# Performance work log

Measured on AMD Instinct MI355X. Metric: run time of the kernel, lower is better.

Reference implementation:

```python
import jax, jax.numpy as jnp
import numpy as np

N = 10000      # atoms
E = 160000     # edges (avg degree 16)
H = 64         # hidden_channels
R = 64         # num_rbf
MAXZ = 100
RC = 4.5       # cutoff_upper (cutoff_lower = 0)
LN_EPS = 1e-5


def setup_inputs() -> dict:
    key = jax.random.key(0)
    ks = jax.random.split(key, 20)
    z = jax.random.randint(ks[0], (N,), 0, MAXZ, dtype=jnp.int32)
    edge_index = jax.random.randint(ks[1], (2, E), 0, N, dtype=jnp.int32)
    edge_weight = jax.random.uniform(ks[2], (E,), dtype=jnp.float32) * RC
    v = jax.random.normal(ks[3], (E, 3), dtype=jnp.float32)
    edge_vec_norm = v / jnp.linalg.norm(v, axis=-1, keepdims=True)
    edge_attr = jax.random.normal(ks[4], (E, R), dtype=jnp.float32)
    p = lambda k, shape: (jax.random.normal(k, shape, dtype=jnp.float32) * 0.1)
    return {
        'z': z, 'edge_index': edge_index, 'edge_weight': edge_weight,
        'edge_vec_norm': edge_vec_norm, 'edge_attr': edge_attr,
        'emb': p(ks[5], (MAXZ, H)),
        'emb2_w': p(ks[6], (H, 2 * H)), 'emb2_b': p(ks[7], (H,)),
        'dp1_w': p(ks[8], (H, R)), 'dp1_b': p(ks[9], (H,)),
        'dp2_w': p(ks[10], (H, R)), 'dp2_b': p(ks[11], (H,)),
        'dp3_w': p(ks[12], (H, R)), 'dp3_b': p(ks[13], (H,)),
        'ln_g': jnp.ones((H,), jnp.float32), 'ln_b': jnp.zeros((H,), jnp.float32),
        'w1': p(ks[14], (2 * H, H)), 'b1': jnp.zeros((2 * H,), jnp.float32),
        'w2': p(ks[15], (3 * H, 2 * H)), 'b2': jnp.zeros((3 * H,), jnp.float32),
        'm0': p(ks[16], (H, H)), 'm1': p(ks[17], (H, H)), 'm2': p(ks[18], (H, H)),
    }


def reference(z, edge_index, edge_weight, edge_vec_norm, edge_attr,
              emb, emb2_w, emb2_b, dp1_w, dp1_b, dp2_w, dp2_b, dp3_w, dp3_b,
              ln_g, ln_b, w1, b1, w2, b2, m0, m1, m2):
    n_atoms = z.shape[0]
    hc = emb.shape[1]
    src, dst = edge_index[0], edge_index[1]

    # atomic number message Z_ij: concat(Z_i, Z_j) -> Linear  [E,H]
    Zn = emb[z]
    Zij = jnp.concatenate([Zn[src], Zn[dst]], axis=-1) @ emb2_w.T + emb2_b

    # cosine cutoff (cutoff_lower == 0)
    C = 0.5 * (jnp.cos(edge_weight * jnp.pi / RC) + 1.0) * (edge_weight < RC)

    # RBF-gated per-edge channel weights, all [E,H]
    g1 = (edge_attr @ dp1_w.T + dp1_b) * C[:, None] * Zij
    g2 = (edge_attr @ dp2_w.T + dp2_b) * C[:, None] * Zij
    g3 = (edge_attr @ dp3_w.T + dp3_b) * C[:, None] * Zij

    eye = jnp.eye(3, dtype=Zij.dtype)
    vx, vy, vz = edge_vec_norm[:, 0], edge_vec_norm[:, 1], edge_vec_norm[:, 2]
    zero = jnp.zeros_like(vx)
    skew = jnp.stack([zero, -vz, vy, vz, zero, -vx, -vy, vx, zero], axis=-1).reshape(-1, 3, 3)
    outer = edge_vec_norm[:, :, None] * edge_vec_norm[:, None, :]  # [E,3,3], symmetric
    sym = outer - (jnp.trace(outer, axis1=-2, axis2=-1) / 3.0)[:, None, None] * eye

    # per-edge messages [E,H,3,3]
    Iij = g1[:, :, None, None] * eye
    Aij = g2[:, :, None, None] * skew[:, None, :, :]
    Sij = g3[:, :, None, None] * sym[:, None, :, :]

    # scatter-add to atoms
    I = jax.ops.segment_sum(Iij, src, num_segments=n_atoms)
    A = jax.ops.segment_sum(Aij, src, num_segments=n_atoms)
    S = jax.ops.segment_sum(Sij, src, num_segments=n_atoms)

    # tensor norm -> layernorm -> MLP1
    tn = ((I + A + S) ** 2).sum((-2, -1))  # [N,H]
    mu = tn.mean(-1, keepdims=True)
    var = ((tn - mu) ** 2).mean(-1, keepdims=True)
    norm = (tn - mu) / jnp.sqrt(var + LN_EPS) * ln_g + ln_b
    norm = jax.nn.silu(norm @ w1.T + b1)
    norm = jax.nn.silu(norm @ w2.T + b2)
    norm = norm.reshape(-1, hc, 3)
    n0 = norm[..., 0][:, :, None, None]

    # channel-mixing; NOTE: original code applies MLP2[1]/MLP2[2] to the
    # updated I and gates all three with norm[...,0] -- replicated faithfully.
    I = jnp.einsum('nhij,kh->nkij', I, m0) * n0
    A = jnp.einsum('nhij,kh->nkij', I, m1) * n0
    S = jnp.einsum('nhij,kh->nkij', I, m2) * n0
    return I + A + S
```

## Files before the change

kernel.cpp:

```cpp
#include <hip/hip_runtime.h>
#include <stdint.h>

#define NATOMS 10000
#define NEDGES 160000
#define RCUT   4.5f
#define CAP    64
#define ATGRID 1024

#define T_BYTES    ((size_t)NATOMS * 640 * 4)
#define CNT_OFF    (T_BYTES)
#define CNT_BYTES  ((size_t)NATOMS * 4)
#define REC_OFF    (CNT_OFF + CNT_BYTES)
#define REC_BYTES  ((size_t)NATOMS * CAP * 16)
#define EMB_OFF    (REC_OFF + REC_BYTES)
#define EMB_BYTES  ((size_t)100 * 64 * 2)

typedef unsigned short u16;
typedef __bf16 bf16x8 __attribute__((ext_vector_type(8)));
typedef float  f32x4  __attribute__((ext_vector_type(4)));

#define MFMA16(a,b,c) __builtin_amdgcn_mfma_f32_16x16x32_bf16((a),(b),(c),0,0,0)
#define BFMAGIC 0x3F803F80u
#define MSK 0xffff0000u

__device__ __forceinline__ float uf(unsigned int u){ return __uint_as_float(u); }
__device__ __forceinline__ float b2f(u16 u){
  union { unsigned int i; float f; } v; v.i = ((unsigned int)u) << 16; return v.f;
}
__device__ __forceinline__ u16 f2b(float f){
  union { unsigned int i; float f; } v; v.f = f;
  unsigned int b = v.i + 0x7fffu + ((v.i >> 16) & 1u);
  return (u16)(b >> 16);
}
__device__ __forceinline__ float ldf(const void* p, int i, int bf){
  if (bf) return b2f(((const u16*)p)[i]);
  return ((const float*)p)[i];
}
__device__ __forceinline__ bf16x8 ld8bf(const void* p, int i, int bf){
  if (bf) return *(const bf16x8*)((const u16*)p + i);
  const float4* q = (const float4*)((const float*)p + i);
  float4 a = q[0], b = q[1];
  bf16x8 r;
  r[0]=(__bf16)a.x; r[1]=(__bf16)a.y; r[2]=(__bf16)a.z; r[3]=(__bf16)a.w;
  r[4]=(__bf16)b.x; r[5]=(__bf16)b.y; r[6]=(__bf16)b.z; r[7]=(__bf16)b.w;
  return r;
}
__device__ __forceinline__ uint4 ld8pk(const void* p, int i, int bf){
  if (bf) return *(const uint4*)((const u16*)p + i);
  const float4* q = (const float4*)((const float*)p + i);
  float4 a = q[0], b = q[1];
  uint4 r;
  r.x = (unsigned int)f2b(a.x) | ((unsigned int)f2b(a.y) << 16);
  r.y = (unsigned int)f2b(a.z) | ((unsigned int)f2b(a.w) << 16);
  r.z = (unsigned int)f2b(b.x) | ((unsigned int)f2b(b.y) << 16);
  r.w = (unsigned int)f2b(b.z) | ((unsigned int)f2b(b.w) << 16);
  return r;
}
__device__ __forceinline__ void ld8f(const void* p, int i, float* o, int bf){
  if (bf){
    uint4 v = *(const uint4*)((const u16*)p + i);
    o[0]=uf(v.x<<16); o[1]=uf(v.x&MSK); o[2]=uf(v.y<<16); o[3]=uf(v.y&MSK);
    o[4]=uf(v.z<<16); o[5]=uf(v.z&MSK); o[6]=uf(v.w<<16); o[7]=uf(v.w&MSK);
    return;
  }
  const float4* q = (const float4*)((const float*)p + i);
  float4 a = q[0], b = q[1];
  o[0]=a.x; o[1]=a.y; o[2]=a.z; o[3]=a.w; o[4]=b.x; o[5]=b.y; o[6]=b.z; o[7]=b.w;
}
__device__ __forceinline__ uint4 pk8(const float* f){
  uint4 r;
  r.x = (unsigned int)f2b(f[0]) | ((unsigned int)f2b(f[1]) << 16);
  r.y = (unsigned int)f2b(f[2]) | ((unsigned int)f2b(f[3]) << 16);
  r.z = (unsigned int)f2b(f[4]) | ((unsigned int)f2b(f[5]) << 16);
  r.w = (unsigned int)f2b(f[6]) | ((unsigned int)f2b(f[7]) << 16);
  return r;
}

__global__ __launch_bounds__(256) void scatter_kernel(const int* __restrict__ ei,
                                                      const int* __restrict__ z,
                                                      const void* __restrict__ ew,
                                                      const void* __restrict__ evn,
                                                      const void* __restrict__ emb,
                                                      u16* __restrict__ emb16,
                                                      int* __restrict__ cnt,
                                                      uint4* __restrict__ REC,
                                                      const unsigned int* __restrict__ lng){
  const int bf = (lng[0] == BFMAGIC);
  int e = blockIdx.x * 256 + threadIdx.x;
  if (e < 6400) emb16[e] = bf ? ((const u16*)emb)[e] : f2b(((const float*)emb)[e]);
  int s = ei[e], d = ei[NEDGES + e];
  int p = atomicAdd(&cnt[s], 1);
  const float w  = ldf(ew, e, bf);
  const float Cv = (w < RCUT) ? 0.5f*(__cosf(w * (3.14159265358979f / RCUT)) + 1.0f) : 0.0f;
  uint4 rec;
  rec.x = (unsigned int)e;
  rec.y = (unsigned int)z[d];
  rec.z = (unsigned int)f2b(ldf(evn, 3*e + 0, bf)) | ((unsigned int)f2b(ldf(evn, 3*e + 1, bf)) << 16);
  rec.w = (unsigned int)f2b(ldf(evn, 3*e + 2, bf)) | ((unsigned int)f2b(Cv) << 16);
  if (p < CAP) REC[(size_t)s*CAP + p] = rec;
}

__global__ __launch_bounds__(256)
void atomT_kernel(
    const int* __restrict__ z,
    const u16* __restrict__ emb16,
    const void* __restrict__ attr,
    const uint4* __restrict__ REC,
    const int* __restrict__ cnt,
    const void* __restrict__ e2w, const void* __restrict__ e2b,
    const void* __restrict__ d1w, const void* __restrict__ d1b,
    const void* __restrict__ d2w, const void* __restrict__ d2b,
    const void* __restrict__ d3w, const void* __restrict__ d3b,
    float* __restrict__ T,
    const unsigned int* __restrict__ lng)
{
  __shared__ __align__(16) u16 dpW[3][64][64];
  __shared__ __align__(16) u16 e2W[64][128];

  const int bf  = (lng[0] == BFMAGIC);
  const int tid = threadIdx.x;
  const void* dps[3] = {d1w, d2w, d3w};
  for (int idx = tid; idx < 1536; idx += 256){
    int w = idx >> 9, rem = idx & 511, r = rem >> 3, c8 = rem & 7;
    *(bf16x8*)&dpW[w][r][(c8 ^ (r & 7))*8] = ld8bf(dps[w], r*64 + c8*8, bf);
  }
  for (int idx = tid; idx < 1024; idx += 256){
    int r = idx >> 4, c8 = idx & 15;
    *(bf16x8*)&e2W[r][(c8 ^ (r & 7))*8] = ld8bf(e2w, r*128 + c8*8, bf);
  }
  __syncthreads();

  const int lane = tid & 63;
  const int wave = tid >> 6;
  const int hh   = lane & 15;
  const int quad = lane >> 4;
  const int half = wave & 1;
  const int ntb  = half * 2;
  const int wpair = wave >> 1;

  float be2[2], bd1[2], bd2[2], bd3[2];
#pragma unroll
  for (int j = 0; j < 2; j++){
    int h = hh + 16*(ntb + j);
    be2[j] = ldf(e2b, h, bf); bd1[j] = ldf(d1b, h, bf);
    bd2[j] = ldf(d2b, h, bf); bd3[j] = ldf(d3b, h, bf);
  }

  int pr  = blockIdx.x;
  int n   = pr * 2 + wpair;
  int cn  = cnt[n];
  int zsv = z[n];

  while (true) {
    const int e0   = n * CAP;
    const int nv   = min(cn, CAP);
    const int e1   = e0 + nv;
    const int e1m1 = (nv > 0) ? (e1 - 1) : e0;
    uint4 recA = REC[min(e0 + hh, e1m1)];

    bf16x8 zf0 = *(const bf16x8*)(emb16 + zsv*64 + quad*8);
    bf16x8 zf1 = *(const bf16x8*)(emb16 + zsv*64 + 32 + quad*8);

    const int prn  = pr + ATGRID;
    const bool more = (prn < NATOMS/2);
    const int nn   = prn * 2 + wpair;
    if (more){ cn = cnt[nn]; zsv = z[nn]; }

    float P[10][2];
#pragma unroll
    for (int c = 0; c < 10; c++){ P[c][0] = 0.f; P[c][1] = 0.f; }

    for (int base = e0; base < e1; base += 16){
      uint4 recN = REC[min(base + 16 + hh, e1m1)];

      bf16x8 af0 = ld8bf(attr, (int)recA.x*64 + quad*8, bf);
      bf16x8 af1 = ld8bf(attr, (int)recA.x*64 + 32 + quad*8, bf);
      bf16x8 zf2 = *(const bf16x8*)(emb16 + recA.y*64 + quad*8);
      bf16x8 zf3 = *(const bf16x8*)(emb16 + recA.y*64 + 32 + quad*8);

      f32x4 aZ[2], a1[2], a2[2], a3[2];
#pragma unroll
      for (int j = 0; j < 2; j++){
        aZ[j] = (f32x4){0.f,0.f,0.f,0.f};
        a1[j] = (f32x4){0.f,0.f,0.f,0.f};
        a2[j] = (f32x4){0.f,0.f,0.f,0.f};
        a3[j] = (f32x4){0.f,0.f,0.f,0.f};
      }

#pragma unroll
      for (int j = 0; j < 2; j++){
        const int h  = hh + 16*(ntb + j);
        const int s0 = (quad       ^ (h & 7)) * 8;
        const int s1 = ((quad + 4) ^ (h & 7)) * 8;
        bf16x8 b;
        b = *(const bf16x8*)&dpW[0][h][s0];           a1[j] = MFMA16(af0, b, a1[j]);
        b = *(const bf16x8*)&dpW[0][h][s1];           a1[j] = MFMA16(af1, b, a1[j]);
        b = *(const bf16x8*)&dpW[1][h][s0];           a2[j] = MFMA16(af0, b, a2[j]);
        b = *(const bf16x8*)&dpW[1][h][s1];           a2[j] = MFMA16(af1, b, a2[j]);
        b = *(const bf16x8*)&dpW[2][h][s0];           a3[j] = MFMA16(af0, b, a3[j]);
        b = *(const bf16x8*)&dpW[2][h][s1];           a3[j] = MFMA16(af1, b, a3[j]);
        b = *(const bf16x8*)&e2W[h][s0];              aZ[j] = MFMA16(zf0, b, aZ[j]);
        b = *(const bf16x8*)&e2W[h][s1];              aZ[j] = MFMA16(zf1, b, aZ[j]);
        b = *(const bf16x8*)&e2W[h][((quad + 8)  ^ (h & 7)) * 8];  aZ[j] = MFMA16(zf2, b, aZ[j]);
        b = *(const bf16x8*)&e2W[h][((quad + 12) ^ (h & 7)) * 8];  aZ[j] = MFMA16(zf3, b, aZ[j]);
      }

#pragma unroll
      for (int r = 0; r < 4; r++){
        const int ii = base + quad*4 + r;
        const bool ea = (ii < e1);
        const int srcl = quad*20 + r;
        const unsigned int rz = (unsigned int)__shfl((int)recA.z, srcl, 64);
        const unsigned int rw = (unsigned int)__shfl((int)recA.w, srcl, 64);
        const float Cv = ea ? b2f((u16)(rw >> 16)) : 0.f;
        const float vx = b2f((u16)(rz & 0xffffu));
        const float vy = b2f((u16)(rz >> 16));
        const float vz = b2f((u16)(rw & 0xffffu));
        const float xx = vx*vx - (1.f/3.f), yy = vy*vy - (1.f/3.f), zz = vz*vz - (1.f/3.f);
        const float xy = vx*vy, xz = vx*vz, yz = vy*vz;
#pragma unroll
        for (int j = 0; j < 2; j++){
          const float czv = Cv * (aZ[j][r] + be2[j]);
          const float g1 = (a1[j][r] + bd1[j]) * czv;
          const float g2 = (a2[j][r] + bd2[j]) * czv;
          const float g3 = (a3[j][r] + bd3[j]) * czv;
          P[0][j] += g1;
          P[1][j] += g2*vx; P[2][j] += g2*vy; P[3][j] += g2*vz;
          P[4][j] += g3*xx; P[5][j] += g3*yy; P[6][j] += g3*zz;
          P[7][j] += g3*xy; P[8][j] += g3*xz; P[9][j] += g3*yz;
        }
      }
      recA = recN;
    }

#pragma unroll
    for (int c = 0; c < 10; c++)
#pragma unroll
      for (int j = 0; j < 2; j++){
        float v = P[c][j];
        v += __shfl_xor(v, 16, 64);
        v += __shfl_xor(v, 32, 64);
        P[c][j] = v;
      }

    if ((quad >> 1) == half){
      float* Tn = T + (size_t)n * 640;
#pragma unroll
      for (int c = 0; c < 10; c++)
        Tn[c*64 + lane] = P[c][quad & 1];
    }

    if (!more) break;
    pr = prn; n = nn;
  }
}

__global__ __launch_bounds__(256) void mlp_kernel(
    const float* __restrict__ T,
    const void* __restrict__ ln_g, const void* __restrict__ ln_b,
    const void* __restrict__ w1,  const void* __restrict__ b1,
    const void* __restrict__ w2,  const void* __restrict__ b2p,
    const void* __restrict__ m0,  const void* __restrict__ m1,
    const void* __restrict__ m2,  void* __restrict__ out,
    const unsigned int* __restrict__ lng)
{
  __shared__ __align__(16) u16 w1L[128][72];
  __shared__ __align__(16) u16 w2L[64][136];
  __shared__ __align__(16) u16 m0L[64][72];
  __shared__ __align__(16) u16 msL[64][72];
  __shared__ __align__(16) float xbuf[4][64];
  __shared__ __align__(16) float hbuf2[4][128];
  __shared__ __align__(16) float isoB[4][64];
  __shared__ __align__(16) float i1B[4][64];

  const int bf  = (lng[0] == BFMAGIC);
  const int tid = threadIdx.x;

  for (int idx = tid; idx < 1024; idx += 256){
    int r = idx >> 3, c8 = idx & 7;
    *(uint4*)&w1L[r][c8*8] = ld8pk(w1, r*64 + c8*8, bf);
  }
  for (int idx = tid; idx < 1024; idx += 256){
    int r = idx >> 4, c8 = idx & 15;
    *(uint4*)&w2L[r][c8*8] = ld8pk(w2, (3*r)*128 + c8*8, bf);
  }
  for (int idx = tid; idx < 512; idx += 256){
    int r = idx >> 3, c8 = idx & 7;
    *(uint4*)&m0L[r][c8*8] = ld8pk(m0, r*64 + c8*8, bf);
    float f[8], g[8];
    ld8f(m1, r*64 + c8*8, f, bf);
    ld8f(m2, r*64 + c8*8, g, bf);
#pragma unroll
    for (int q = 0; q < 8; q++) f[q] += g[q];
    *(uint4*)&msL[r][c8*8] = pk8(f);
  }
  __syncthreads();

  const int wave = tid >> 6;
  const int h    = tid & 63;
  const int wid  = blockIdx.x * 4 + wave;

  const float lngh = ldf(ln_g, h, bf), lnbh = ldf(ln_b, h, bf);
  const float b1a = ldf(b1, h, bf), b1b = ldf(b1, h + 64, bf);
  const float b2h = ldf(b2p, 3*h, bf);

  const uint4*  A4 = (const uint4*)&w1L[h][0];
  const uint4*  B4 = (const uint4*)&w1L[h + 64][0];
  const uint4*  W4 = (const uint4*)&w2L[h][0];
  const uint4*  M4 = (const uint4*)&m0L[h][0];
  const uint4*  S4 = (const uint4*)&msL[h][0];
  const float4* X4  = (const float4*)&xbuf[wave][0];
  const float4* H4  = (const float4*)&hbuf2[wave][0];
  const float4* I4  = (const float4*)&isoB[wave][0];
  const float4* J4  = (const float4*)&i1B[wave][0];

  const int NITER = (NATOMS + 2047) / 2048;
  for (int it = 0; it < NITER; it++){
    const int n   = wid + it * 2048;
    const bool act = (n < NATOMS);
    const int na  = act ? n : 0;

    const float* Tn = T + (size_t)na * 640;
    const float iso = Tn[h];
    const float wx = Tn[64+h], wy = Tn[128+h], wz = Tn[192+h];
    const float sxx = Tn[256+h], syy = Tn[320+h], szz = Tn[384+h];
    const float sxy = Tn[448+h], sxz = Tn[512+h], syz = Tn[576+h];
    const float tn = (iso+sxx)*(iso+sxx) + (iso+syy)*(iso+syy) + (iso+szz)*(iso+szz)
                   + 2.f*(sxy*sxy + sxz*sxz + syz*syz + wx*wx + wy*wy + wz*wz);
    isoB[wave][h] = iso;

    float s = tn;
#pragma unroll
    for (int off = 32; off; off >>= 1) s += __shfl_xor(s, off, 64);
    const float mu = s * (1.f/64.f);
    const float d0 = tn - mu;
    float v = d0 * d0;
#pragma unroll
    for (int off = 32; off; off >>= 1) v += __shfl_xor(v, off, 64);
    v *= (1.f/64.f);
    xbuf[wave][h] = d0 * rsqrtf(v + 1e-5f) * lngh + lnbh;
    __syncthreads();

    float acc0 = b1a, acc1 = b1b;
#pragma unroll
    for (int q = 0; q < 8; q++){
      const uint4 A = A4[q], B = B4[q];
      const float4 x0 = X4[2*q], x1 = X4[2*q + 1];
      acc0 += uf(A.x << 16)*x0.x + uf(A.x & MSK)*x0.y;
      acc0 += uf(A.y << 16)*x0.z + uf(A.y & MSK)*x0.w;
      acc0 += uf(A.z << 16)*x1.x + uf(A.z & MSK)*x1.y;
      acc0 += uf(A.w << 16)*x1.z + uf(A.w & MSK)*x1.w;
      acc1 += uf(B.x << 16)*x0.x + uf(B.x & MSK)*x0.y;
      acc1 += uf(B.y << 16)*x0.z + uf(B.y & MSK)*x0.w;
      acc1 += uf(B.z << 16)*x1.x + uf(B.z & MSK)*x1.y;
      acc1 += uf(B.w << 16)*x1.z + uf(B.w & MSK)*x1.w;
    }
    acc0 = acc0 / (1.f + __expf(-acc0));
    acc1 = acc1 / (1.f + __expf(-acc1));
    hbuf2[wave][h] = acc0; hbuf2[wave][h + 64] = acc1;
    __syncthreads();

    float acc2 = b2h, t1 = 0.f;
#pragma unroll
    for (int q = 0; q < 16; q++){
      const uint4 W = W4[q];
      const float4 y0 = H4[2*q], y1 = H4[2*q + 1];
      acc2 += uf(W.x << 16)*y0.x + uf(W.x & MSK)*y0.y;
      acc2 += uf(W.y << 16)*y0.z + uf(W.y & MSK)*y0.w;
      acc2 += uf(W.z << 16)*y1.x + uf(W.z & MSK)*y1.y;
      acc2 += uf(W.w << 16)*y1.z + uf(W.w & MSK)*y1.w;
    }
#pragma unroll
    for (int q = 0; q < 8; q++){
      const uint4 M = M4[q];
      const float4 x0 = I4[2*q], x1 = I4[2*q + 1];
      t1 += uf(M.x << 16)*x0.x + uf(M.x & MSK)*x0.y;
      t1 += uf(M.y << 16)*x0.z + uf(M.y & MSK)*x0.w;
      t1 += uf(M.z << 16)*x1.x + uf(M.z & MSK)*x1.y;
      t1 += uf(M.w << 16)*x1.z + uf(M.w & MSK)*x1.w;
    }
    const float n0 = acc2 / (1.f + __expf(-acc2));
    const float iso1 = t1 * n0;
    i1B[wave][h] = iso1;
    __syncthreads();

    float t23 = 0.f;
#pragma unroll
    for (int q = 0; q < 8; q++){
      const uint4 M = S4[q];
      const float4 x0 = J4[2*q], x1 = J4[2*q + 1];
      t23 += uf(M.x << 16)*x0.x + uf(M.x & MSK)*x0.y;
      t23 += uf(M.y << 16)*x0.z + uf(M.y & MSK)*x0.w;
      t23 += uf(M.z << 16)*x1.x + uf(M.z & MSK)*x1.y;
      t23 += uf(M.w << 16)*x1.z + uf(M.w & MSK)*x1.w;
    }
    const float dval = iso1 + t23 * n0;

    if (act){
      if (bf){
        u16* o = (u16*)out + (size_t)n * 576 + h * 9;
        const u16 db = f2b(dval);
        o[0] = db; o[1] = 0; o[2] = 0;
        o[3] = 0;  o[4] = db; o[5] = 0;
        o[6] = 0;  o[7] = 0;  o[8] = db;
      } else {
        float* o = (float*)out + (size_t)n * 576 + h * 9;
        o[0] = dval; o[1] = 0.f; o[2] = 0.f;
        o[3] = 0.f;  o[4] = dval; o[5] = 0.f;
        o[6] = 0.f;  o[7] = 0.f;  o[8] = dval;
      }
    }
    __syncthreads();
  }
}

extern "C" void kernel_launch(void* const* d_in, const int* in_sizes, int n_in,
                              void* d_out, int out_size, void* d_ws, size_t ws_size,
                              hipStream_t stream) {
  const int* z    = (const int*)d_in[0];
  const int* ei   = (const int*)d_in[1];
  const void* ew   = d_in[2];
  const void* evn  = d_in[3];
  const void* attr = d_in[4];
  const void* emb  = d_in[5];
  const void* e2w  = d_in[6];
  const void* e2b  = d_in[7];
  const void* d1w  = d_in[8];
  const void* d1b  = d_in[9];
  const void* d2w  = d_in[10];
  const void* d2b  = d_in[11];
  const void* d3w  = d_in[12];
  const void* d3b  = d_in[13];
  const void* ln_g = d_in[14];
  const void* ln_b = d_in[15];
  const void* w1   = d_in[16];
  const void* b1   = d_in[17];
  const void* w2   = d_in[18];
  const void* b2p  = d_in[19];
  const void* m0   = d_in[20];
  const void* m1   = d_in[21];
  const void* m2   = d_in[22];
  const unsigned int* lng = (const unsigned int*)ln_g;

  char* ws = (char*)d_ws;
  float*   T     = (float*)ws;
  int*     cnt   = (int*)(ws + CNT_OFF);
  uint4*   REC   = (uint4*)(ws + REC_OFF);
  u16*     emb16 = (u16*)(ws + EMB_OFF);

  hipMemsetAsync(cnt, 0, CNT_BYTES, stream);
  scatter_kernel<<<NEDGES/256, 256, 0, stream>>>(ei, z, ew, evn, emb, emb16, cnt, REC, lng);
  atomT_kernel<<<ATGRID, 256, 0, stream>>>(z, emb16, attr, REC, cnt, e2w, e2b,
                                           d1w, d1b, d2w, d2b, d3w, d3b, T, lng);
  mlp_kernel<<<512, 256, 0, stream>>>(T, ln_g, ln_b, w1, b1, w2, b2p,
                                      m0, m1, m2, d_out, lng);
}
```

Before: 234.5 us.

## Software-pipeline edge attribute and embedding gathers one chunk and one atom ahead

Restructures the per-atom edge loop so the gathered edge_attr rows and neighbor embeddings for the next 16-edge chunk are loaded while the current chunk's MFMAs run. The first chunk of the next atom is also prefetched before the current atom's reductions and stores. The atom-list metadata (counts, z) is now fetched two atoms ahead. The aim is to hide global-memory gather latency behind compute, at the cost of more live registers. Indices are clamped so the speculative loads stay in bounds.

```diff
diff --git a/kernel.cpp b/kernel.cpp
--- a/kernel.cpp
+++ b/kernel.cpp
@@ -146,37 +146,57 @@
     bd2[j] = ldf(d2b, h, bf); bd3[j] = ldf(d3b, h, bf);
   }
 
+  const int NPAIR = NATOMS / 2;
+  const unsigned EMAX = (unsigned)(NEDGES - 1);
+
   int pr  = blockIdx.x;
   int n   = pr * 2 + wpair;
-  int cn  = cnt[n];
-  int zsv = z[n];
+  int cnA = cnt[n];
+  int zA  = z[n];
+
+  int prB    = pr + ATGRID;
+  bool moreB = (prB < NPAIR);
+  int nB     = moreB ? (prB * 2 + wpair) : n;
+  int cnB    = cnt[nB];
+  int zB     = z[nB];
+
+  int e0 = n * CAP;
+  int nv = min(cnA, CAP);
+  uint4 recA = REC[e0 + min((int)hh, max(nv - 1, 0))];
+
+  bf16x8 af0, af1, zf2, zf3;
+  {
+    const int ex = (int)min(recA.x, EMAX);
+    af0 = ld8bf(attr, ex*64 + quad*8, bf);
+    af1 = ld8bf(attr, ex*64 + 32 + quad*8, bf);
+    const int ey = (int)min(recA.y, 99u);
+    zf2 = *(const bf16x8*)(emb16 + ey*64 + quad*8);
+    zf3 = *(const bf16x8*)(emb16 + ey*64 + 32 + quad*8);
+  }
 
   while (true) {
-    const int e0   = n * CAP;
-    const int nv   = min(cn, CAP);
-    const int e1   = e0 + nv;
-    const int e1m1 = (nv > 0) ? (e1 - 1) : e0;
-    uint4 recA = REC[min(e0 + hh, e1m1)];
-
-    bf16x8 zf0 = *(const bf16x8*)(emb16 + zsv*64 + quad*8);
-    bf16x8 zf1 = *(const bf16x8*)(emb16 + zsv*64 + 32 + quad*8);
-
-    const int prn  = pr + ATGRID;
-    const bool more = (prn < NATOMS/2);
-    const int nn   = prn * 2 + wpair;
-    if (more){ cn = cnt[nn]; zsv = z[nn]; }
+    const int e1 = e0 + nv;
+
+    const int e0B = nB * CAP;
+    const int nvB = min(cnB, CAP);
+    uint4 recB = REC[e0B + min((int)hh, max(nvB - 1, 0))];
+
+    const int prC   = prB + ATGRID;
+    const bool moreC = (prC < NPAIR);
+    const int nC    = moreC ? (prC * 2 + wpair) : nB;
+    const int cnC   = cnt[nC];
+    const int zC    = z[nC];
+
+    bf16x8 zf0 = *(const bf16x8*)(emb16 + zA*64 + quad*8);
+    bf16x8 zf1 = *(const bf16x8*)(emb16 + zA*64 + 32 + quad*8);
 
     float P[10][2];
 #pragma unroll
     for (int c = 0; c < 10; c++){ P[c][0] = 0.f; P[c][1] = 0.f; }
 
     for (int base = e0; base < e1; base += 16){
-      uint4 recN = REC[min(base + 16 + hh, e1m1)];
-
-      bf16x8 af0 = ld8bf(attr, (int)recA.x*64 + quad*8, bf);
-      bf16x8 af1 = ld8bf(attr, (int)recA.x*64 + 32 + quad*8, bf);
-      bf16x8 zf2 = *(const bf16x8*)(emb16 + recA.y*64 + quad*8);
-      bf16x8 zf3 = *(const bf16x8*)(emb16 + recA.y*64 + 32 + quad*8);
+      const bool lastC = (base + 16 >= e1);
+      uint4 recN = REC[min(base + 16 + hh, e1 - 1)];
 
       f32x4 aZ[2], a1[2], a2[2], a3[2];
 #pragma unroll
@@ -205,6 +225,16 @@
         b = *(const bf16x8*)&e2W[h][((quad + 12) ^ (h & 7)) * 8];  aZ[j] = MFMA16(zf3, b, aZ[j]);
       }
 
+      bf16x8 afN0, afN1, zfN2, zfN3;
+      if (!lastC){
+        const int ex = (int)min(recN.x, EMAX);
+        afN0 = ld8bf(attr, ex*64 + quad*8, bf);
+        afN1 = ld8bf(attr, ex*64 + 32 + quad*8, bf);
+        const int ey = (int)min(recN.y, 99u);
+        zfN2 = *(const bf16x8*)(emb16 + ey*64 + quad*8);
+        zfN3 = *(const bf16x8*)(emb16 + ey*64 + 32 + quad*8);
+      }
+
 #pragma unroll
       for (int r = 0; r < 4; r++){
         const int ii = base + quad*4 + r;
@@ -230,7 +260,17 @@
           P[7][j] += g3*xy; P[8][j] += g3*xz; P[9][j] += g3*yz;
         }
       }
-      recA = recN;
+
+      if (!lastC){ recA = recN; af0 = afN0; af1 = afN1; zf2 = zfN2; zf3 = zfN3; }
+    }
+
+    {
+      const int ex = (int)min(recB.x, EMAX);
+      af0 = ld8bf(attr, ex*64 + quad*8, bf);
+      af1 = ld8bf(attr, ex*64 + 32 + quad*8, bf);
+      const int ey = (int)min(recB.y, 99u);
+      zf2 = *(const bf16x8*)(emb16 + ey*64 + quad*8);
+      zf3 = *(const bf16x8*)(emb16 + ey*64 + 32 + quad*8);
     }
 
 #pragma unroll
@@ -250,8 +290,9 @@
         Tn[c*64 + lane] = P[c][quad & 1];
     }
 
-    if (!more) break;
-    pr = prn; n = nn;
+    if (!moreB) break;
+    pr = prB; n = nB; zA = zB; e0 = e0B; nv = nvB; recA = recB;
+    prB = prC; moreB = moreC; nB = nC; cnB = cnC; zB = zC;
   }
 }
 
```

Measured after the change: 277.8 us. 18.4% more time.

## Pre-sort edge RBF features into per-atom contiguous bf16 buffer during scatter

Applied to the files above, without the earlier changes.

The scatter kernel now also copies each edge's 64-wide edge_attr row, converted to bf16, into a per-source-atom bucketed buffer. A new atomT_stream kernel reads these rows contiguously instead of gathering them by edge id, which replaces random gathers with streaming reads in the main per-atom kernel. The cost is an extra write of roughly 80 MB of workspace (mostly padding capacity) plus a scattered write in the scatter kernel. The new path runs only when the workspace is large enough, otherwise it falls back to the old kernel.

```diff
diff --git a/kernel.cpp b/kernel.cpp
--- a/kernel.cpp
+++ b/kernel.cpp
@@ -14,6 +14,9 @@
 #define REC_BYTES  ((size_t)NATOMS * CAP * 16)
 #define EMB_OFF    (REC_OFF + REC_BYTES)
 #define EMB_BYTES  ((size_t)100 * 64 * 2)
+#define ATTR2_OFF  (EMB_OFF + 0x4000)
+#define ATTR2_BYTES ((size_t)NATOMS * CAP * 64 * 2)
+#define WS_NEED    (ATTR2_OFF + ATTR2_BYTES)
 
 typedef unsigned short u16;
 typedef __bf16 bf16x8 __attribute__((ext_vector_type(8)));
@@ -84,6 +87,8 @@
                                                       u16* __restrict__ emb16,
                                                       int* __restrict__ cnt,
                                                       uint4* __restrict__ REC,
+                                                      const void* __restrict__ attr,
+                                                      u16* __restrict__ attr2,
                                                       const unsigned int* __restrict__ lng){
   const int bf = (lng[0] == BFMAGIC);
   int e = blockIdx.x * 256 + threadIdx.x;
@@ -97,7 +102,172 @@
   rec.y = (unsigned int)z[d];
   rec.z = (unsigned int)f2b(ldf(evn, 3*e + 0, bf)) | ((unsigned int)f2b(ldf(evn, 3*e + 1, bf)) << 16);
   rec.w = (unsigned int)f2b(ldf(evn, 3*e + 2, bf)) | ((unsigned int)f2b(Cv) << 16);
-  if (p < CAP) REC[(size_t)s*CAP + p] = rec;
+  if (p < CAP){
+    REC[(size_t)s*CAP + p] = rec;
+    if (attr2){
+      u16* dst = attr2 + ((size_t)s*CAP + p)*64;
+#pragma unroll
+      for (int k = 0; k < 8; k++)
+        *(uint4*)(dst + k*8) = ld8pk(attr, e*64 + k*8, bf);
+    }
+  }
+}
+
+__global__ __launch_bounds__(256)
+void atomT_stream(
+    const int* __restrict__ z,
+    const u16* __restrict__ emb16,
+    const u16* __restrict__ attr2,
+    const uint4* __restrict__ REC,
+    const int* __restrict__ cnt,
+    const void* __restrict__ e2w, const void* __restrict__ e2b,
+    const void* __restrict__ d1w, const void* __restrict__ d1b,
+    const void* __restrict__ d2w, const void* __restrict__ d2b,
+    const void* __restrict__ d3w, const void* __restrict__ d3b,
+    float* __restrict__ T,
+    const unsigned int* __restrict__ lng)
+{
+  __shared__ __align__(16) u16 dpW[3][64][64];
+  __shared__ __align__(16) u16 e2W[64][128];
+
+  const int bf  = (lng[0] == BFMAGIC);
+  const int tid = threadIdx.x;
+  const void* dps[3] = {d1w, d2w, d3w};
+  for (int idx = tid; idx < 1536; idx += 256){
+    int w = idx >> 9, rem = idx & 511, r = rem >> 3, c8 = rem & 7;
+    *(bf16x8*)&dpW[w][r][(c8 ^ (r & 7))*8] = ld8bf(dps[w], r*64 + c8*8, bf);
+  }
+  for (int idx = tid; idx < 1024; idx += 256){
+    int r = idx >> 4, c8 = idx & 15;
+    *(bf16x8*)&e2W[r][(c8 ^ (r & 7))*8] = ld8bf(e2w, r*128 + c8*8, bf);
+  }
+  __syncthreads();
+
+  const int lane = tid & 63;
+  const int wave = tid >> 6;
+  const int hh   = lane & 15;
+  const int quad = lane >> 4;
+  const int half = wave & 1;
+  const int ntb  = half * 2;
+  const int wpair = wave >> 1;
+
+  float be2[2], bd1[2], bd2[2], bd3[2];
+#pragma unroll
+  for (int j = 0; j < 2; j++){
+    int h = hh + 16*(ntb + j);
+    be2[j] = ldf(e2b, h, bf); bd1[j] = ldf(d1b, h, bf);
+    bd2[j] = ldf(d2b, h, bf); bd3[j] = ldf(d3b, h, bf);
+  }
+
+  int pr  = blockIdx.x;
+  int n   = pr * 2 + wpair;
+  int cn  = cnt[n];
+  int zsv = z[n];
+
+  while (true) {
+    const int e0   = n * CAP;
+    const int nv   = min(cn, CAP);
+    const int e1   = e0 + nv;
+    const int e1m1 = (nv > 0) ? (e1 - 1) : e0;
+    uint4 recA = REC[min(e0 + hh, e1m1)];
+
+    bf16x8 zf0 = *(const bf16x8*)(emb16 + zsv*64 + quad*8);
+    bf16x8 zf1 = *(const bf16x8*)(emb16 + zsv*64 + 32 + quad*8);
+
+    const int prn  = pr + ATGRID;
+    const bool more = (prn < NATOMS/2);
+    const int nn   = prn * 2 + wpair;
+    if (more){ cn = cnt[nn]; zsv = z[nn]; }
+
+    float P[10][2];
+#pragma unroll
+    for (int c = 0; c < 10; c++){ P[c][0] = 0.f; P[c][1] = 0.f; }
+
+    for (int base = e0; base < e1; base += 16){
+      const size_t sA = (size_t)min(base + hh, e1 - 1) * 64;
+      bf16x8 af0 = *(const bf16x8*)(attr2 + sA + quad*8);
+      bf16x8 af1 = *(const bf16x8*)(attr2 + sA + 32 + quad*8);
+
+      uint4 recN = REC[min(base + 16 + hh, e1 - 1)];
+
+      bf16x8 zf2 = *(const bf16x8*)(emb16 + recA.y*64 + quad*8);
+      bf16x8 zf3 = *(const bf16x8*)(emb16 + recA.y*64 + 32 + quad*8);
+
+      f32x4 aZ[2], a1[2], a2[2], a3[2];
+#pragma unroll
+      for (int j = 0; j < 2; j++){
+        aZ[j] = (f32x4){0.f,0.f,0.f,0.f};
+        a1[j] = (f32x4){0.f,0.f,0.f,0.f};
+        a2[j] = (f32x4){0.f,0.f,0.f,0.f};
+        a3[j] = (f32x4){0.f,0.f,0.f,0.f};
+      }
+
+#pragma unroll
+      for (int j = 0; j < 2; j++){
+        const int h  = hh + 16*(ntb + j);
+        const int s0 = (quad       ^ (h & 7)) * 8;
+        const int s1 = ((quad + 4) ^ (h & 7)) * 8;
+        bf16x8 b;
+        b = *(const bf16x8*)&dpW[0][h][s0];           a1[j] = MFMA16(af0, b, a1[j]);
+        b = *(const bf16x8*)&dpW[0][h][s1];           a1[j] = MFMA16(af1, b, a1[j]);
+        b = *(const bf16x8*)&dpW[1][h][s0];           a2[j] = MFMA16(af0, b, a2[j]);
+        b = *(const bf16x8*)&dpW[1][h][s1];           a2[j] = MFMA16(af1, b, a2[j]);
+        b = *(const bf16x8*)&dpW[2][h][s0];           a3[j] = MFMA16(af0, b, a3[j]);
+        b = *(const bf16x8*)&dpW[2][h][s1];           a3[j] = MFMA16(af1, b, a3[j]);
+        b = *(const bf16x8*)&e2W[h][s0];              aZ[j] = MFMA16(zf0, b, aZ[j]);
+        b = *(const bf16x8*)&e2W[h][s1];              aZ[j] = MFMA16(zf1, b, aZ[j]);
+        b = *(const bf16x8*)&e2W[h][((quad + 8)  ^ (h & 7)) * 8];  aZ[j] = MFMA16(zf2, b, aZ[j]);
+        b = *(const bf16x8*)&e2W[h][((quad + 12) ^ (h & 7)) * 8];  aZ[j] = MFMA16(zf3, b, aZ[j]);
+      }
+
+#pragma unroll
+      for (int r = 0; r < 4; r++){
+        const int ii = base + quad*4 + r;
+        const bool ea = (ii < e1);
+        const int srcl = quad*20 + r;
+        const unsigned int rz = (unsigned int)__shfl((int)recA.z, srcl, 64);
+        const unsigned int rw = (unsigned int)__shfl((int)recA.w, srcl, 64);
+        const float Cv = ea ? b2f((u16)(rw >> 16)) : 0.f;
+        const float vx = b2f((u16)(rz & 0xffffu));
+        const float vy = b2f((u16)(rz >> 16));
+        const float vz = b2f((u16)(rw & 0xffffu));
+        const float xx = vx*vx - (1.f/3.f), yy = vy*vy - (1.f/3.f), zz = vz*vz - (1.f/3.f);
+        const float xy = vx*vy, xz = vx*vz, yz = vy*vz;
+#pragma unroll
+        for (int j = 0; j < 2; j++){
+          const float czv = Cv * (aZ[j][r] + be2[j]);
+          const float g1 = (a1[j][r] + bd1[j]) * czv;
+          const float g2 = (a2[j][r] + bd2[j]) * czv;
+          const float g3 = (a3[j][r] + bd3[j]) * czv;
+          P[0][j] += g1;
+          P[1][j] += g2*vx; P[2][j] += g2*vy; P[3][j] += g2*vz;
+          P[4][j] += g3*xx; P[5][j] += g3*yy; P[6][j] += g3*zz;
+          P[7][j] += g3*xy; P[8][j] += g3*xz; P[9][j] += g3*yz;
+        }
+      }
+      recA = recN;
+    }
+
+#pragma unroll
+    for (int c = 0; c < 10; c++)
+#pragma unroll
+      for (int j = 0; j < 2; j++){
+        float v = P[c][j];
+        v += __shfl_xor(v, 16, 64);
+        v += __shfl_xor(v, 32, 64);
+        P[c][j] = v;
+      }
+
+    if ((quad >> 1) == half){
+      float* Tn = T + (size_t)n * 640;
+#pragma unroll
+      for (int c = 0; c < 10; c++)
+        Tn[c*64 + lane] = P[c][quad & 1];
+    }
+
+    if (!more) break;
+    pr = prn; n = nn;
+  }
 }
 
 __global__ __launch_bounds__(256)
@@ -171,7 +341,7 @@
     for (int c = 0; c < 10; c++){ P[c][0] = 0.f; P[c][1] = 0.f; }
 
     for (int base = e0; base < e1; base += 16){
-      uint4 recN = REC[min(base + 16 + hh, e1m1)];
+      uint4 recN = REC[min(base + 16 + hh, e1 - 1)];
 
       bf16x8 af0 = ld8bf(attr, (int)recA.x*64 + quad*8, bf);
       bf16x8 af1 = ld8bf(attr, (int)recA.x*64 + 32 + quad*8, bf);
@@ -447,11 +617,17 @@
   int*     cnt   = (int*)(ws + CNT_OFF);
   uint4*   REC   = (uint4*)(ws + REC_OFF);
   u16*     emb16 = (u16*)(ws + EMB_OFF);
+  u16*     attr2 = (ws_size >= WS_NEED) ? (u16*)(ws + ATTR2_OFF) : nullptr;
 
   hipMemsetAsync(cnt, 0, CNT_BYTES, stream);
-  scatter_kernel<<<NEDGES/256, 256, 0, stream>>>(ei, z, ew, evn, emb, emb16, cnt, REC, lng);
-  atomT_kernel<<<ATGRID, 256, 0, stream>>>(z, emb16, attr, REC, cnt, e2w, e2b,
-                                           d1w, d1b, d2w, d2b, d3w, d3b, T, lng);
+  scatter_kernel<<<NEDGES/256, 256, 0, stream>>>(ei, z, ew, evn, emb, emb16, cnt, REC,
+                                                 attr, attr2, lng);
+  if (attr2)
+    atomT_stream<<<ATGRID, 256, 0, stream>>>(z, emb16, attr2, REC, cnt, e2w, e2b,
+                                             d1w, d1b, d2w, d2b, d3w, d3b, T, lng);
+  else
+    atomT_kernel<<<ATGRID, 256, 0, stream>>>(z, emb16, attr, REC, cnt, e2w, e2b,
+                                             d1w, d1b, d2w, d2b, d3w, d3b, T, lng);
   mlp_kernel<<<512, 256, 0, stream>>>(T, ln_g, ln_b, w1, b1, w2, b2p,
                                       m0, m1, m2, d_out, lng);
 }
```

New measurement: 251.0 us. +7.0%, slower.
